# Optimization experiments

Measured on AMD Instinct MI355X. Metric: run time of the kernel, lower is better.

The kernel has to match this reference:

```python
import jax, jax.numpy as jnp
import numpy as np

NUM_ITERS = 3


def squash(s, axis=-1):
    # v = (|s|^2 / (1+|s|^2)) * s / |s|
    sq = jnp.sum(s * s, axis=axis, keepdims=True)
    return sq / (1.0 + sq) * s / jnp.sqrt(sq)


def setup_inputs() -> dict:
    key = jax.random.key(0)
    k1, k2 = jax.random.split(key)
    B, C, R, I, O = 256, 10, 1152, 8, 16
    x = jax.random.normal(k1, (B, R, I), dtype=jnp.float32)
    route_weights = jax.random.normal(k2, (C, R, I, O), dtype=jnp.float32)
    return {"x": x, "route_weights": route_weights}


def reference(x, route_weights):
    # x: [B, R, I]; route_weights: [C, R, I, O]
    # u: predictions from each route node for each output capsule: [B, C, R, 1, O]
    u = jnp.einsum("bri,crio->bcro", x, route_weights)[:, :, :, None, :]
    b = jnp.zeros_like(u)
    v = None
    for i in range(NUM_ITERS):
        c = jax.nn.softmax(b, axis=2)          # softmax over route nodes (dim=2)
        s = jnp.sum(c * u, axis=2, keepdims=True)  # [B, C, 1, 1, O]
        v = squash(s, axis=-1)
        if i != NUM_ITERS - 1:
            b = b + jnp.sum(u * v, axis=-1, keepdims=True)  # agreement, broadcast over O
    return v  # [B, C, 1, 1, O]
```

## Files before the change

### kernel.cpp

```cpp
#include <hip/hip_runtime.h>


#define B_ 256
#define C_ 10
#define R_ 1152
#define I_ 8
#define O_ 16
#define T_ 512
#define BPB 2
#define RPP 128
#define KPT 9
#define NW 8
#define NITER 3

__global__ __launch_bounds__(T_, 2) void capsule_routing_kernel(
    const float* __restrict__ x,
    const float* __restrict__ w,
    float* __restrict__ out)
{
    const int c    = blockIdx.x >> 7;
    const int bh   = blockIdx.x & 127;
    const int b0   = bh * BPB;
    const int tid  = threadIdx.x;
    const int lane = tid & 63;
    const int wid  = tid >> 6;
    const int oq   = tid & 3;
    const int rl   = tid >> 2;

    __shared__ float sred[BPB][NW][4][4];
    __shared__ float zred[BPB][NW];
    __shared__ float vfin[BPB][O_];

    float u0[KPT][4], u1[KPT][4];
    float lg0[KPT], lg1[KPT];

    #pragma unroll
    for (int k = 0; k < KPT; ++k) {
        const int r = k * RPP + rl;
        const float4* xp0 = (const float4*)(x + ((size_t)b0 * R_ + r) * I_);
        const float4 xa0 = xp0[0];
        const float4 xb0 = xp0[1];
        const float4* xp1 = (const float4*)(x + ((size_t)(b0 + 1) * R_ + r) * I_);
        const float4 xa1 = xp1[0];
        const float4 xb1 = xp1[1];
        const float xs0[8] = {xa0.x, xa0.y, xa0.z, xa0.w, xb0.x, xb0.y, xb0.z, xb0.w};
        const float xs1[8] = {xa1.x, xa1.y, xa1.z, xa1.w, xb1.x, xb1.y, xb1.z, xb1.w};
        const float* wp = w + ((size_t)c * R_ + r) * (I_ * O_) + oq * 4;
        float4 a0 = make_float4(0.f, 0.f, 0.f, 0.f);
        float4 a1 = make_float4(0.f, 0.f, 0.f, 0.f);
        #pragma unroll
        for (int i = 0; i < I_; ++i) {
            const float4 wv = *(const float4*)(wp + i * O_);
            a0.x += xs0[i] * wv.x;  a1.x += xs1[i] * wv.x;
            a0.y += xs0[i] * wv.y;  a1.y += xs1[i] * wv.y;
            a0.z += xs0[i] * wv.z;  a1.z += xs1[i] * wv.z;
            a0.w += xs0[i] * wv.w;  a1.w += xs1[i] * wv.w;
        }
        u0[k][0] = a0.x; u0[k][1] = a0.y; u0[k][2] = a0.z; u0[k][3] = a0.w;
        u1[k][0] = a1.x; u1[k][1] = a1.y; u1[k][2] = a1.z; u1[k][3] = a1.w;
        lg0[k] = 0.f;
        lg1[k] = 0.f;
    }

    for (int it = 0; it < NITER; ++it) {
        float z0 = 0.f, z1 = 0.f;
        float s00 = 0.f, s01 = 0.f, s02 = 0.f, s03 = 0.f;
        float s10 = 0.f, s11 = 0.f, s12 = 0.f, s13 = 0.f;
        #pragma unroll
        for (int k = 0; k < KPT; ++k) {
            const float e0 = __expf(lg0[k]);
            z0 += e0;
            s00 += e0 * u0[k][0]; s01 += e0 * u0[k][1];
            s02 += e0 * u0[k][2]; s03 += e0 * u0[k][3];
            const float e1 = __expf(lg1[k]);
            z1 += e1;
            s10 += e1 * u1[k][0]; s11 += e1 * u1[k][1];
            s12 += e1 * u1[k][2]; s13 += e1 * u1[k][3];
        }
        #pragma unroll
        for (int off = 4; off <= 32; off <<= 1) {
            z0 += __shfl_xor(z0, off);   z1 += __shfl_xor(z1, off);
            s00 += __shfl_xor(s00, off); s01 += __shfl_xor(s01, off);
            s02 += __shfl_xor(s02, off); s03 += __shfl_xor(s03, off);
            s10 += __shfl_xor(s10, off); s11 += __shfl_xor(s11, off);
            s12 += __shfl_xor(s12, off); s13 += __shfl_xor(s13, off);
        }
        if (lane < 4) {
            sred[0][wid][lane][0] = s00; sred[0][wid][lane][1] = s01;
            sred[0][wid][lane][2] = s02; sred[0][wid][lane][3] = s03;
            sred[1][wid][lane][0] = s10; sred[1][wid][lane][1] = s11;
            sred[1][wid][lane][2] = s12; sred[1][wid][lane][3] = s13;
            if (lane == 0) { zred[0][wid] = z0; zred[1][wid] = z1; }
        }
        __syncthreads();

        if (wid == 0 && lane < 2 * O_) {
            const int bb = lane >> 4;
            const int o  = lane & 15;
            float S = 0.f, Z = 0.f;
            #pragma unroll
            for (int wv = 0; wv < NW; ++wv) {
                S += sred[bb][wv][o >> 2][o & 3];
                Z += zred[bb][wv];
            }
            float p = S * S;
            p += __shfl_xor(p, 1);
            p += __shfl_xor(p, 2);
            p += __shfl_xor(p, 4);
            p += __shfl_xor(p, 8);
            const float inv = 1.f / Z;
            const float svn = S * inv;
            const float sqn = p * inv * inv;
            const float scale = sqrtf(sqn) / (1.f + sqn);
            const float vf = svn * scale;
            vfin[bb][o] = vf;
            if (it == NITER - 1)
                out[((size_t)(b0 + bb) * C_ + c) * O_ + o] = vf;
        }

        if (it != NITER - 1) {
            __syncthreads();
            const float4 v0 = *(const float4*)&vfin[0][oq * 4];
            const float4 v1 = *(const float4*)&vfin[1][oq * 4];
            #pragma unroll
            for (int k = 0; k < KPT; ++k) {
                float d0 = u0[k][0] * v0.x + u0[k][1] * v0.y +
                           u0[k][2] * v0.z + u0[k][3] * v0.w;
                float d1 = u1[k][0] * v1.x + u1[k][1] * v1.y +
                           u1[k][2] * v1.z + u1[k][3] * v1.w;
                d0 += __shfl_xor(d0, 1);
                d0 += __shfl_xor(d0, 2);
                d1 += __shfl_xor(d1, 1);
                d1 += __shfl_xor(d1, 2);
                lg0[k] += d0;
                lg1[k] += d1;
            }
        }
    }
}

extern "C" void kernel_launch(void* const* d_in, const int* in_sizes, int n_in,
                              void* d_out, int out_size, void* d_ws, size_t ws_size,
                              hipStream_t stream) {
    const float* x = (const float*)d_in[0];
    const float* w = (const float*)d_in[1];
    float* out = (float*)d_out;
    capsule_routing_kernel<<<dim3(C_ * (B_ / BPB)), dim3(T_), 0, stream>>>(x, w, out);
}
```

Before: 73.61 us.

## Split output dims over 8 lanes, recompute logits from summed v, remap XCDs

```diff
diff --git a/kernel.cpp b/kernel.cpp
--- a/kernel.cpp
+++ b/kernel.cpp
@@ -6,33 +6,38 @@
 #define R_ 1152
 #define I_ 8
 #define O_ 16
-#define T_ 512
+#define T_ 1024
 #define BPB 2
+#define GRP 8
 #define RPP 128
 #define KPT 9
-#define NW 8
+#define NW 16
 #define NITER 3
+#define NXCD 8
 
 __global__ __launch_bounds__(T_, 2) void capsule_routing_kernel(
     const float* __restrict__ x,
     const float* __restrict__ w,
     float* __restrict__ out)
 {
-    const int c    = blockIdx.x >> 7;
-    const int bh   = blockIdx.x & 127;
+    const int wg = (blockIdx.x & (NXCD - 1)) * (C_ * (B_ / BPB) / NXCD)
+                 + (blockIdx.x >> 3);
+    const int c    = wg >> 7;
+    const int bh   = wg & 127;
     const int b0   = bh * BPB;
     const int tid  = threadIdx.x;
     const int lane = tid & 63;
     const int wid  = tid >> 6;
-    const int oq   = tid & 3;
-    const int rl   = tid >> 2;
+    const int g    = tid & 7;
+    const int rl   = tid >> 3;
 
-    __shared__ float sred[BPB][NW][4][4];
+    __shared__ float sred[BPB][NW][GRP][2];
     __shared__ float zred[BPB][NW];
-    __shared__ float vfin[BPB][O_];
+    __shared__ float vsum[BPB][O_];
 
-    float u0[KPT][4], u1[KPT][4];
-    float lg0[KPT], lg1[KPT];
+    float u0[KPT][2], u1[KPT][2];
+
+    if (tid < BPB * O_) vsum[tid >> 4][tid & 15] = 0.f;
 
     #pragma unroll
     for (int k = 0; k < KPT; ++k) {
@@ -45,51 +50,45 @@
         const float4 xb1 = xp1[1];
         const float xs0[8] = {xa0.x, xa0.y, xa0.z, xa0.w, xb0.x, xb0.y, xb0.z, xb0.w};
         const float xs1[8] = {xa1.x, xa1.y, xa1.z, xa1.w, xb1.x, xb1.y, xb1.z, xb1.w};
-        const float* wp = w + ((size_t)c * R_ + r) * (I_ * O_) + oq * 4;
-        float4 a0 = make_float4(0.f, 0.f, 0.f, 0.f);
-        float4 a1 = make_float4(0.f, 0.f, 0.f, 0.f);
+        const float* wp = w + ((size_t)c * R_ + r) * (I_ * O_) + g * 2;
+        float a00 = 0.f, a01 = 0.f, a10 = 0.f, a11 = 0.f;
         #pragma unroll
         for (int i = 0; i < I_; ++i) {
-            const float4 wv = *(const float4*)(wp + i * O_);
-            a0.x += xs0[i] * wv.x;  a1.x += xs1[i] * wv.x;
-            a0.y += xs0[i] * wv.y;  a1.y += xs1[i] * wv.y;
-            a0.z += xs0[i] * wv.z;  a1.z += xs1[i] * wv.z;
-            a0.w += xs0[i] * wv.w;  a1.w += xs1[i] * wv.w;
+            const float2 wv = *(const float2*)(wp + i * O_);
+            a00 += xs0[i] * wv.x;  a01 += xs0[i] * wv.y;
+            a10 += xs1[i] * wv.x;  a11 += xs1[i] * wv.y;
         }
-        u0[k][0] = a0.x; u0[k][1] = a0.y; u0[k][2] = a0.z; u0[k][3] = a0.w;
-        u1[k][0] = a1.x; u1[k][1] = a1.y; u1[k][2] = a1.z; u1[k][3] = a1.w;
-        lg0[k] = 0.f;
-        lg1[k] = 0.f;
+        u0[k][0] = a00; u0[k][1] = a01;
+        u1[k][0] = a10; u1[k][1] = a11;
     }
+    __syncthreads();
 
     for (int it = 0; it < NITER; ++it) {
+        const float2 vs0 = *(const float2*)&vsum[0][g * 2];
+        const float2 vs1 = *(const float2*)&vsum[1][g * 2];
         float z0 = 0.f, z1 = 0.f;
-        float s00 = 0.f, s01 = 0.f, s02 = 0.f, s03 = 0.f;
-        float s10 = 0.f, s11 = 0.f, s12 = 0.f, s13 = 0.f;
+        float s00 = 0.f, s01 = 0.f, s10 = 0.f, s11 = 0.f;
         #pragma unroll
         for (int k = 0; k < KPT; ++k) {
-            const float e0 = __expf(lg0[k]);
-            z0 += e0;
-            s00 += e0 * u0[k][0]; s01 += e0 * u0[k][1];
-            s02 += e0 * u0[k][2]; s03 += e0 * u0[k][3];
-            const float e1 = __expf(lg1[k]);
-            z1 += e1;
-            s10 += e1 * u1[k][0]; s11 += e1 * u1[k][1];
-            s12 += e1 * u1[k][2]; s13 += e1 * u1[k][3];
+            float d0 = u0[k][0] * vs0.x + u0[k][1] * vs0.y;
+            float d1 = u1[k][0] * vs1.x + u1[k][1] * vs1.y;
+            d0 += __shfl_xor(d0, 1); d1 += __shfl_xor(d1, 1);
+            d0 += __shfl_xor(d0, 2); d1 += __shfl_xor(d1, 2);
+            d0 += __shfl_xor(d0, 4); d1 += __shfl_xor(d1, 4);
+            const float e0 = __expf(d0);
+            const float e1 = __expf(d1);
+            z0 += e0;  s00 += e0 * u0[k][0];  s01 += e0 * u0[k][1];
+            z1 += e1;  s10 += e1 * u1[k][0];  s11 += e1 * u1[k][1];
         }
         #pragma unroll
-        for (int off = 4; off <= 32; off <<= 1) {
+        for (int off = 8; off <= 32; off <<= 1) {
             z0 += __shfl_xor(z0, off);   z1 += __shfl_xor(z1, off);
             s00 += __shfl_xor(s00, off); s01 += __shfl_xor(s01, off);
-            s02 += __shfl_xor(s02, off); s03 += __shfl_xor(s03, off);
             s10 += __shfl_xor(s10, off); s11 += __shfl_xor(s11, off);
-            s12 += __shfl_xor(s12, off); s13 += __shfl_xor(s13, off);
         }
-        if (lane < 4) {
+        if (lane < GRP) {
             sred[0][wid][lane][0] = s00; sred[0][wid][lane][1] = s01;
-            sred[0][wid][lane][2] = s02; sred[0][wid][lane][3] = s03;
             sred[1][wid][lane][0] = s10; sred[1][wid][lane][1] = s11;
-            sred[1][wid][lane][2] = s12; sred[1][wid][lane][3] = s13;
             if (lane == 0) { zred[0][wid] = z0; zred[1][wid] = z1; }
         }
         __syncthreads();
@@ -100,42 +99,23 @@
             float S = 0.f, Z = 0.f;
             #pragma unroll
             for (int wv = 0; wv < NW; ++wv) {
-                S += sred[bb][wv][o >> 2][o & 3];
+                S += sred[bb][wv][o >> 1][o & 1];
                 Z += zred[bb][wv];
             }
-            float p = S * S;
+            const float inv = 1.f / Z;
+            const float svn = S * inv;
+            float p = svn * svn;
             p += __shfl_xor(p, 1);
             p += __shfl_xor(p, 2);
             p += __shfl_xor(p, 4);
             p += __shfl_xor(p, 8);
-            const float inv = 1.f / Z;
-            const float svn = S * inv;
-            const float sqn = p * inv * inv;
-            const float scale = sqrtf(sqn) / (1.f + sqn);
+            const float scale = sqrtf(p) / (1.f + p);
             const float vf = svn * scale;
-            vfin[bb][o] = vf;
+            vsum[bb][o] += vf;
             if (it == NITER - 1)
                 out[((size_t)(b0 + bb) * C_ + c) * O_ + o] = vf;
         }
-
-        if (it != NITER - 1) {
-            __syncthreads();
-            const float4 v0 = *(const float4*)&vfin[0][oq * 4];
-            const float4 v1 = *(const float4*)&vfin[1][oq * 4];
-            #pragma unroll
-            for (int k = 0; k < KPT; ++k) {
-                float d0 = u0[k][0] * v0.x + u0[k][1] * v0.y +
-                           u0[k][2] * v0.z + u0[k][3] * v0.w;
-                float d1 = u1[k][0] * v1.x + u1[k][1] * v1.y +
-                           u1[k][2] * v1.z + u1[k][3] * v1.w;
-                d0 += __shfl_xor(d0, 1);
-                d0 += __shfl_xor(d0, 2);
-                d1 += __shfl_xor(d1, 1);
-                d1 += __shfl_xor(d1, 2);
-                lg0[k] += d0;
-                lg1[k] += d1;
-            }
-        }
+        if (it != NITER - 1) __syncthreads();
     }
 }
 
```

Measured after the change: 127.6 us. 73.4% more time.
